# Kernel optimization log

Measured on AMD Instinct MI355X. Metric: run time of the kernel, lower is better.

The kernel has to match this reference:

```python
import jax, jax.numpy as jnp
import numpy as np

N_NODES = 50000
N_EDGES = 1600000


def setup_inputs() -> dict:
    key = jax.random.key(0)
    k1, k2, k3, k4 = jax.random.split(key, 4)
    x = jax.random.normal(k1, (N_NODES, 256), dtype=jnp.float32)
    edge_index = jax.random.randint(k2, (2, N_EDGES), 0, N_NODES, dtype=jnp.int64)
    W1 = jax.random.normal(k3, (256, 128), dtype=jnp.float32) * 0.05
    b1 = jnp.zeros((128,), dtype=jnp.float32)
    Wc = jax.random.normal(k4, (128, 10), dtype=jnp.float32) * 0.05
    bc = jnp.zeros((10,), dtype=jnp.float32)
    return {"x": x, "edge_index": edge_index, "W1": W1, "b1": b1,
            "Wc": Wc, "bc": bc, "conv_time": 30}


def reference(x, edge_index, W1, b1, Wc, bc, conv_time):
    """GCNConv(num_features->nhid) with conv_time propagation hops, ReLU, Linear cls."""
    n = x.shape[0]
    # linear transform first (standard GCNConv: transform then propagate)
    h = x @ W1 + b1  # [N, nhid]
    # add self-loops (GCN default)
    loop = jnp.arange(n, dtype=edge_index.dtype)
    src = jnp.concatenate([edge_index[0], loop])
    dst = jnp.concatenate([edge_index[1], loop])
    # symmetric normalization D^{-1/2} A_hat D^{-1/2}
    deg = jax.ops.segment_sum(jnp.ones_like(dst, dtype=h.dtype), dst, num_segments=n)
    dinv = jax.lax.rsqrt(jnp.maximum(deg, 1.0))
    norm = (dinv[src] * dinv[dst])[:, None]  # [E+N, 1]

    def hop(i, h):
        msg = h[src] * norm                      # gather + scale
        return jax.ops.segment_sum(msg, dst, num_segments=n)  # scatter-add

    h = jax.lax.fori_loop(0, conv_time, hop, h)
    h = jax.nn.relu(h)
    return h @ Wc + bc  # [N, num_classes]
```

## Files before the change

### kernel.cpp

```cpp
#include <hip/hip_runtime.h>
#include <hip/hip_bf16.h>

#define NFEAT 256
#define NHID  128
#define NCLS  10
#define CONV_TIME 30
#define NSLICE 8
#define SFEAT  16

__global__ void deg_kernel(const int* __restrict__ ei, int* __restrict__ cnt, int E) {
    int e = blockIdx.x * blockDim.x + threadIdx.x;
    if (e < E) {
        int d = ei[(size_t)E + e];
        atomicAdd(&cnt[d], 1);
    }
}

__global__ void dinv_kernel(const int* __restrict__ cnt, float* __restrict__ dinv, int n) {
    int i = blockIdx.x * blockDim.x + threadIdx.x;
    if (i < n) {
        float deg = (float)(cnt[i] + 1);
        dinv[i] = 1.0f / sqrtf(deg);
    }
}

__global__ void alloc_kernel(const int* __restrict__ cnt, int* __restrict__ alloc,
                             int* __restrict__ pbeg, int* __restrict__ plen,
                             int* __restrict__ pos, int n) {
    int i    = blockIdx.x * blockDim.x + threadIdx.x;
    int lane = threadIdx.x & 63;
    int pl   = 0;
    if (i < n) pl = (cnt[i] + 7) & ~7;
    int v = pl;
#pragma unroll
    for (int d = 1; d < 64; d <<= 1) {
        int t = __shfl_up(v, d, 64);
        if (lane >= d) v += t;
    }
    int total = __shfl(v, 63, 64);
    int excl  = v - pl;
    int base  = 0;
    if (lane == 63) base = atomicAdd(alloc, total);
    base = __shfl(base, 63, 64);
    if (i < n) {
        int seg = base + excl;
        pbeg[i] = seg;
        plen[i] = pl;
        pos[i]  = seg;
    }
}

__global__ void fill_esrc_kernel(unsigned int* __restrict__ esrc32, unsigned int val, int nwords) {
    int i = blockIdx.x * blockDim.x + threadIdx.x;
    if (i < nwords) esrc32[i] = val;
}

__global__ void scatter_kernel(const int* __restrict__ ei, int* __restrict__ pos,
                               unsigned short* __restrict__ esrc, int E) {
    int e = blockIdx.x * blockDim.x + threadIdx.x;
    if (e < E) {
        int s = ei[e];
        int d = ei[(size_t)E + e];
        int p = atomicAdd(&pos[d], 1);
        esrc[p] = (unsigned short)s;
    }
}

__global__ void init_dummy_kernel(float* __restrict__ hA, float* __restrict__ hB,
                                  int n, int np1) {
    int t = threadIdx.x;
    if (t < NSLICE * SFEAT) {
        int sl = t >> 4, f = t & 15;
        size_t idx = (size_t)sl * np1 * SFEAT + (size_t)n * SFEAT + f;
        hA[idx] = 0.0f;
        hB[idx] = 0.0f;
    }
}

__global__ __launch_bounds__(256) void gemm1_kernel(const float* __restrict__ x,
                                                    const float* __restrict__ W1,
                                                    const float* __restrict__ b1,
                                                    const float* __restrict__ dinv,
                                                    float* __restrict__ g, int M, int np1) {
    __shared__ float As[64][20];
    __shared__ float Bs[16][128];
    int tid = threadIdx.x;
    int m0  = blockIdx.x * 64;
    int tx  = tid & 15;
    int ty  = tid >> 4;
    int ar  = tid >> 2, aq = tid & 3;
    int br  = tid >> 4, bc = tid & 15;

    float acc[4][8];
#pragma unroll
    for (int i = 0; i < 4; ++i)
#pragma unroll
        for (int j = 0; j < 8; ++j) acc[i][j] = 0.0f;

    for (int kb = 0; kb < NFEAT; kb += 16) {
        float4 av = make_float4(0.f, 0.f, 0.f, 0.f);
        int arow = m0 + ar;
        if (arow < M) av = *(const float4*)(x + (size_t)arow * NFEAT + kb + aq * 4);
        *(float4*)&As[ar][aq * 4] = av;
        *(float4*)&Bs[br][bc * 8]     = *(const float4*)(W1 + (size_t)(kb + br) * NHID + bc * 8);
        *(float4*)&Bs[br][bc * 8 + 4] = *(const float4*)(W1 + (size_t)(kb + br) * NHID + bc * 8 + 4);
        __syncthreads();
#pragma unroll
        for (int k = 0; k < 16; ++k) {
            float a0 = As[ty * 4 + 0][k];
            float a1 = As[ty * 4 + 1][k];
            float a2 = As[ty * 4 + 2][k];
            float a3 = As[ty * 4 + 3][k];
            float4 b0 = *(float4*)&Bs[k][tx * 8];
            float4 b1v = *(float4*)&Bs[k][tx * 8 + 4];
            float bv[8] = {b0.x, b0.y, b0.z, b0.w, b1v.x, b1v.y, b1v.z, b1v.w};
            float avv[4] = {a0, a1, a2, a3};
#pragma unroll
            for (int i = 0; i < 4; ++i)
#pragma unroll
                for (int j = 0; j < 8; ++j)
                    acc[i][j] = fmaf(avv[i], bv[j], acc[i][j]);
        }
        __syncthreads();
    }
    int col0 = tx * 8;
    int sl   = col0 >> 4;
    int c0   = col0 & 15;
#pragma unroll
    for (int i = 0; i < 4; ++i) {
        int row = m0 + ty * 4 + i;
        if (row < M) {
            float dv = dinv[row];
            float* dst = g + (size_t)sl * np1 * SFEAT + (size_t)row * SFEAT + c0;
#pragma unroll
            for (int j = 0; j < 8; ++j)
                dst[j] = dv * (acc[i][j] + b1[col0 + j]);
        }
    }
}

__global__ __launch_bounds__(256) void hop_kernel(const float* __restrict__ gin,
                                                  float* __restrict__ gout,
                                                  const int* __restrict__ pbeg,
                                                  const int* __restrict__ plen,
                                                  const unsigned short* __restrict__ esrc,
                                                  const float* __restrict__ dinv,
                                                  int n, int np1, int last) {
    int bid  = blockIdx.x;
    int sl   = bid & (NSLICE - 1);
    int grp  = (bid >> 3) * 4 + (threadIdx.x >> 6);
    if (grp * 16 >= n) return;
    int lane = threadIdx.x & 63;
    int slot = lane >> 2;
    int fl   = lane & 3;
    int node = grp * 16 + slot;
    bool valid = node < n;
    int nodeC = valid ? node : n;
    const float4* __restrict__ gs4 = (const float4*)(gin + (size_t)sl * np1 * SFEAT);
    float4*       __restrict__ go4 = (float4*)(gout + (size_t)sl * np1 * SFEAT);

    int beg = 0, L = 0;
    if (valid) { beg = pbeg[node]; L = plen[node]; }

    float4 acc = make_float4(0.f, 0.f, 0.f, 0.f);
    const uint4* __restrict__ e4 = (const uint4*)esrc;
    for (int i = 0; i < L; i += 8) {
        uint4 w = e4[(beg + i) >> 3];
        int s0 = w.x & 0xFFFF, s1 = w.x >> 16;
        int s2 = w.y & 0xFFFF, s3 = w.y >> 16;
        int s4 = w.z & 0xFFFF, s5 = w.z >> 16;
        int s6 = w.w & 0xFFFF, s7 = w.w >> 16;
        float4 v0 = gs4[(size_t)s0 * 4 + fl];
        float4 v1 = gs4[(size_t)s1 * 4 + fl];
        float4 v2 = gs4[(size_t)s2 * 4 + fl];
        float4 v3 = gs4[(size_t)s3 * 4 + fl];
        float4 v4 = gs4[(size_t)s4 * 4 + fl];
        float4 v5 = gs4[(size_t)s5 * 4 + fl];
        float4 v6 = gs4[(size_t)s6 * 4 + fl];
        float4 v7 = gs4[(size_t)s7 * 4 + fl];
        acc.x += v0.x + v1.x + v2.x + v3.x + v4.x + v5.x + v6.x + v7.x;
        acc.y += v0.y + v1.y + v2.y + v3.y + v4.y + v5.y + v6.y + v7.y;
        acc.z += v0.z + v1.z + v2.z + v3.z + v4.z + v5.z + v6.z + v7.z;
        acc.w += v0.w + v1.w + v2.w + v3.w + v4.w + v5.w + v6.w + v7.w;
    }
    float4 sf = gs4[(size_t)nodeC * 4 + fl];
    acc.x += sf.x; acc.y += sf.y; acc.z += sf.z; acc.w += sf.w;
    float dv = valid ? dinv[node] : 1.0f;
    float sc = last ? dv : dv * dv;
    acc.x *= sc; acc.y *= sc; acc.z *= sc; acc.w *= sc;
    if (valid) go4[(size_t)node * 4 + fl] = acc;
}

__global__ __launch_bounds__(256) void cls_kernel(const float* __restrict__ h,
                                                  const float* __restrict__ Wc,
                                                  const float* __restrict__ bc,
                                                  float* __restrict__ out, int n, int np1) {
    __shared__ float wc[NHID * NCLS];
    __shared__ float bcs[NCLS];
    int tid = threadIdx.x;
    for (int i = tid; i < NHID * NCLS; i += 256) wc[i] = Wc[i];
    if (tid < NCLS) bcs[tid] = bc[tid];
    __syncthreads();
    int i = blockIdx.x * 256 + tid;
    if (i >= n) return;
    float acc[NCLS];
#pragma unroll
    for (int c = 0; c < NCLS; ++c) acc[c] = bcs[c];
#pragma unroll
    for (int s = 0; s < NSLICE; ++s) {
        const float4* hr = (const float4*)(h + ((size_t)s * np1 + i) * SFEAT);
#pragma unroll
        for (int q = 0; q < 4; ++q) {
            float4 v = hr[q];
            float vs[4] = {fmaxf(v.x, 0.f), fmaxf(v.y, 0.f), fmaxf(v.z, 0.f), fmaxf(v.w, 0.f)};
#pragma unroll
            for (int j = 0; j < 4; ++j)
#pragma unroll
                for (int c = 0; c < NCLS; ++c)
                    acc[c] = fmaf(vs[j], wc[(s * SFEAT + q * 4 + j) * NCLS + c], acc[c]);
        }
    }
#pragma unroll
    for (int c = 0; c < NCLS; ++c) out[(size_t)i * NCLS + c] = acc[c];
}

static inline size_t align256(size_t x) { return (x + 255) & ~(size_t)255; }

extern "C" void kernel_launch(void* const* d_in, const int* in_sizes, int n_in,
                              void* d_out, int out_size, void* d_ws, size_t ws_size,
                              hipStream_t stream) {
    const float* x   = (const float*)d_in[0];
    const int*   ei  = (const int*)d_in[1];
    const float* W1  = (const float*)d_in[2];
    const float* b1  = (const float*)d_in[3];
    const float* Wc  = (const float*)d_in[4];
    const float* bc  = (const float*)d_in[5];
    float*       out = (float*)d_out;

    const int N    = in_sizes[0] / NFEAT;
    const int E    = in_sizes[1] / 2;
    const int NP1  = N + 1;
    const int EPAD = E + 8 * N + 64;

    char* ws = (char*)d_ws;
    size_t off = 0;
    float*          hA   = (float*)(ws + off); off = align256(off + (size_t)NSLICE * NP1 * SFEAT * 4);
    float*          hB   = (float*)(ws + off); off = align256(off + (size_t)NSLICE * NP1 * SFEAT * 4);
    int*            cnt  = (int*)  (ws + off); off = align256(off + (size_t)(N + 64) * 4);
    float*          dinv = (float*)(ws + off); off = align256(off + (size_t)N * 4);
    int*            pbeg = (int*)  (ws + off); off = align256(off + (size_t)N * 4);
    int*            plen = (int*)  (ws + off); off = align256(off + (size_t)N * 4);
    int*            pos  = (int*)  (ws + off); off = align256(off + (size_t)N * 4);
    unsigned short* esrc = (unsigned short*)(ws + off); off = align256(off + (size_t)EPAD * 2);
    int*            alloc = cnt + N;

    hipMemsetAsync(cnt, 0, (size_t)(N + 64) * 4, stream);

    deg_kernel<<<(E + 255) / 256, 256, 0, stream>>>(ei, cnt, E);
    dinv_kernel<<<(N + 255) / 256, 256, 0, stream>>>(cnt, dinv, N);
    alloc_kernel<<<(N + 255) / 256, 256, 0, stream>>>(cnt, alloc, pbeg, plen, pos, N);
    {
        unsigned int v = ((unsigned)N << 16) | (unsigned)N;
        int nwords = EPAD / 2;
        fill_esrc_kernel<<<(nwords + 255) / 256, 256, 0, stream>>>((unsigned int*)esrc, v, nwords);
    }
    scatter_kernel<<<(E + 255) / 256, 256, 0, stream>>>(ei, pos, esrc, E);
    init_dummy_kernel<<<1, 256, 0, stream>>>(hA, hB, N, NP1);

    gemm1_kernel<<<(N + 63) / 64, 256, 0, stream>>>(x, W1, b1, dinv, hA, N, NP1);

    int ngrp = (N + 15) / 16;
    int hop_blocks = NSLICE * ((ngrp + 3) / 4);
    for (int i = 0; i < CONV_TIME; ++i) {
        const float* gi = (i & 1) ? hB : hA;
        float*       go = (i & 1) ? hA : hB;
        hop_kernel<<<hop_blocks, 256, 0, stream>>>(gi, go, pbeg, plen, esrc, dinv, N, NP1,
                                                   (i == CONV_TIME - 1) ? 1 : 0);
    }

    cls_kernel<<<(N + 255) / 256, 256, 0, stream>>>(hA, Wc, bc, out, N, NP1);
}
```

Before: 2.446 ms.

## Renumber nodes by degree bucket and partition degree/scatter atomics by destination range

Nodes are sorted into buckets by padded in-degree, and the feature buffers, CSR metadata and edge source indices are renumbered into this sorted order. The goal is that the 16 nodes sharing a wavefront in the hop kernel have similar neighbour counts, which cuts loop divergence and idle lanes across the 30 propagation hops. The final classifier writes each row back to its original node index. Separately, the degree and scatter kernels now launch 8x the blocks, and each block handles only destinations in one eighth of the node range, to localise atomics. This costs extra passes over the edge list and several small preprocessing kernels.

```diff
diff --git a/kernel.cpp b/kernel.cpp
--- a/kernel.cpp
+++ b/kernel.cpp
@@ -7,12 +7,16 @@
 #define CONV_TIME 30
 #define NSLICE 8
 #define SFEAT  16
-
-__global__ void deg_kernel(const int* __restrict__ ei, int* __restrict__ cnt, int E) {
-    int e = blockIdx.x * blockDim.x + threadIdx.x;
+#define NBUCK  32
+
+__global__ void deg_kernel(const int* __restrict__ ei, int* __restrict__ cnt, int E, int n) {
+    int part = blockIdx.x & 7;
+    int e = (blockIdx.x >> 3) * blockDim.x + threadIdx.x;
+    int lo = (int)(((long long)part * n) >> 3);
+    int hi = (int)(((long long)(part + 1) * n) >> 3);
     if (e < E) {
         int d = ei[(size_t)E + e];
-        atomicAdd(&cnt[d], 1);
+        if (d >= lo && d < hi) atomicAdd(&cnt[d], 1);
     }
 }
 
@@ -50,19 +54,84 @@
     }
 }
 
+__global__ void hist_kernel(const int* __restrict__ plen, int* __restrict__ bcnt, int n) {
+    __shared__ int lh[NBUCK];
+    int tid = threadIdx.x;
+    if (tid < NBUCK) lh[tid] = 0;
+    __syncthreads();
+    int i = blockIdx.x * blockDim.x + tid;
+    if (i < n) {
+        int b = min(plen[i] >> 3, NBUCK - 1);
+        atomicAdd(&lh[b], 1);
+    }
+    __syncthreads();
+    if (tid < NBUCK && lh[tid]) atomicAdd(&bcnt[tid], lh[tid]);
+}
+
+__global__ void scan32_kernel(const int* __restrict__ bcnt, int* __restrict__ bpos) {
+    if (threadIdx.x == 0) {
+        int a = 0;
+        for (int b = 0; b < NBUCK; ++b) { bpos[b] = a; a += bcnt[b]; }
+    }
+}
+
+__global__ void place_kernel(const int* __restrict__ plen, int* __restrict__ bpos,
+                             int* __restrict__ nperm, int* __restrict__ rank, int n) {
+    int i    = blockIdx.x * blockDim.x + threadIdx.x;
+    int lane = threadIdx.x & 63;
+    int b    = -1;
+    if (i < n) b = min(plen[i] >> 3, NBUCK - 1);
+#pragma unroll 1
+    for (int bb = 0; bb < NBUCK; ++bb) {
+        unsigned long long mask = __ballot(b == bb);
+        if (mask == 0ULL) continue;
+        int leader = __ffsll((unsigned long long)mask) - 1;
+        int cnt    = __popcll(mask);
+        int base   = 0;
+        if (lane == leader) base = atomicAdd(&bpos[bb], cnt);
+        base = __shfl(base, leader, 64);
+        int r = __popcll(mask & ((1ULL << lane) - 1ULL));
+        if (b == bb) {
+            int p = base + r;
+            nperm[p] = i;
+            rank[i]  = p;
+        }
+    }
+}
+
+__global__ void gather_sorted_kernel(const int* __restrict__ nperm,
+                                     const int* __restrict__ pbeg, const int* __restrict__ plen,
+                                     const float* __restrict__ dinv,
+                                     int* __restrict__ pbeg_s, int* __restrict__ plen_s,
+                                     float* __restrict__ dinv_s, int n) {
+    int i = blockIdx.x * blockDim.x + threadIdx.x;
+    if (i < n) {
+        int nd = nperm[i];
+        pbeg_s[i] = pbeg[nd];
+        plen_s[i] = plen[nd];
+        dinv_s[i] = dinv[nd];
+    }
+}
+
 __global__ void fill_esrc_kernel(unsigned int* __restrict__ esrc32, unsigned int val, int nwords) {
     int i = blockIdx.x * blockDim.x + threadIdx.x;
     if (i < nwords) esrc32[i] = val;
 }
 
-__global__ void scatter_kernel(const int* __restrict__ ei, int* __restrict__ pos,
-                               unsigned short* __restrict__ esrc, int E) {
-    int e = blockIdx.x * blockDim.x + threadIdx.x;
+__global__ void scatter_kernel(const int* __restrict__ ei, const int* __restrict__ rank,
+                               int* __restrict__ pos, unsigned short* __restrict__ esrc,
+                               int E, int n) {
+    int part = blockIdx.x & 7;
+    int e = (blockIdx.x >> 3) * blockDim.x + threadIdx.x;
+    int lo = (int)(((long long)part * n) >> 3);
+    int hi = (int)(((long long)(part + 1) * n) >> 3);
     if (e < E) {
-        int s = ei[e];
         int d = ei[(size_t)E + e];
-        int p = atomicAdd(&pos[d], 1);
-        esrc[p] = (unsigned short)s;
+        if (d >= lo && d < hi) {
+            int s = ei[e];
+            int p = atomicAdd(&pos[d], 1);
+            esrc[p] = (unsigned short)rank[s];
+        }
     }
 }
 
@@ -81,6 +150,7 @@
                                                     const float* __restrict__ W1,
                                                     const float* __restrict__ b1,
                                                     const float* __restrict__ dinv,
+                                                    const int* __restrict__ rank,
                                                     float* __restrict__ g, int M, int np1) {
     __shared__ float As[64][20];
     __shared__ float Bs[16][128];
@@ -131,7 +201,8 @@
         int row = m0 + ty * 4 + i;
         if (row < M) {
             float dv = dinv[row];
-            float* dst = g + (size_t)sl * np1 * SFEAT + (size_t)row * SFEAT + c0;
+            int   rk = rank[row];
+            float* dst = g + (size_t)sl * np1 * SFEAT + (size_t)rk * SFEAT + c0;
 #pragma unroll
             for (int j = 0; j < 8; ++j)
                 dst[j] = dv * (acc[i][j] + b1[col0 + j]);
@@ -141,10 +212,10 @@
 
 __global__ __launch_bounds__(256) void hop_kernel(const float* __restrict__ gin,
                                                   float* __restrict__ gout,
-                                                  const int* __restrict__ pbeg,
-                                                  const int* __restrict__ plen,
+                                                  const int* __restrict__ pbeg_s,
+                                                  const int* __restrict__ plen_s,
                                                   const unsigned short* __restrict__ esrc,
-                                                  const float* __restrict__ dinv,
+                                                  const float* __restrict__ dinv_s,
                                                   int n, int np1, int last) {
     int bid  = blockIdx.x;
     int sl   = bid & (NSLICE - 1);
@@ -153,14 +224,14 @@
     int lane = threadIdx.x & 63;
     int slot = lane >> 2;
     int fl   = lane & 3;
-    int node = grp * 16 + slot;
-    bool valid = node < n;
-    int nodeC = valid ? node : n;
+    int idx  = grp * 16 + slot;
+    bool valid = idx < n;
+    int idxC = valid ? idx : n;
     const float4* __restrict__ gs4 = (const float4*)(gin + (size_t)sl * np1 * SFEAT);
     float4*       __restrict__ go4 = (float4*)(gout + (size_t)sl * np1 * SFEAT);
 
     int beg = 0, L = 0;
-    if (valid) { beg = pbeg[node]; L = plen[node]; }
+    if (valid) { beg = pbeg_s[idx]; L = plen_s[idx]; }
 
     float4 acc = make_float4(0.f, 0.f, 0.f, 0.f);
     const uint4* __restrict__ e4 = (const uint4*)esrc;
@@ -183,17 +254,18 @@
         acc.z += v0.z + v1.z + v2.z + v3.z + v4.z + v5.z + v6.z + v7.z;
         acc.w += v0.w + v1.w + v2.w + v3.w + v4.w + v5.w + v6.w + v7.w;
     }
-    float4 sf = gs4[(size_t)nodeC * 4 + fl];
+    float4 sf = gs4[(size_t)idxC * 4 + fl];
     acc.x += sf.x; acc.y += sf.y; acc.z += sf.z; acc.w += sf.w;
-    float dv = valid ? dinv[node] : 1.0f;
+    float dv = valid ? dinv_s[idx] : 1.0f;
     float sc = last ? dv : dv * dv;
     acc.x *= sc; acc.y *= sc; acc.z *= sc; acc.w *= sc;
-    if (valid) go4[(size_t)node * 4 + fl] = acc;
+    if (valid) go4[(size_t)idx * 4 + fl] = acc;
 }
 
 __global__ __launch_bounds__(256) void cls_kernel(const float* __restrict__ h,
                                                   const float* __restrict__ Wc,
                                                   const float* __restrict__ bc,
+                                                  const int* __restrict__ nperm,
                                                   float* __restrict__ out, int n, int np1) {
     __shared__ float wc[NHID * NCLS];
     __shared__ float bcs[NCLS];
@@ -220,8 +292,9 @@
                     acc[c] = fmaf(vs[j], wc[(s * SFEAT + q * 4 + j) * NCLS + c], acc[c]);
         }
     }
-#pragma unroll
-    for (int c = 0; c < NCLS; ++c) out[(size_t)i * NCLS + c] = acc[c];
+    int nd = nperm[i];
+#pragma unroll
+    for (int c = 0; c < NCLS; ++c) out[(size_t)nd * NCLS + c] = acc[c];
 }
 
 static inline size_t align256(size_t x) { return (x + 255) & ~(size_t)255; }
@@ -244,39 +317,53 @@
 
     char* ws = (char*)d_ws;
     size_t off = 0;
-    float*          hA   = (float*)(ws + off); off = align256(off + (size_t)NSLICE * NP1 * SFEAT * 4);
-    float*          hB   = (float*)(ws + off); off = align256(off + (size_t)NSLICE * NP1 * SFEAT * 4);
-    int*            cnt  = (int*)  (ws + off); off = align256(off + (size_t)(N + 64) * 4);
-    float*          dinv = (float*)(ws + off); off = align256(off + (size_t)N * 4);
-    int*            pbeg = (int*)  (ws + off); off = align256(off + (size_t)N * 4);
-    int*            plen = (int*)  (ws + off); off = align256(off + (size_t)N * 4);
-    int*            pos  = (int*)  (ws + off); off = align256(off + (size_t)N * 4);
-    unsigned short* esrc = (unsigned short*)(ws + off); off = align256(off + (size_t)EPAD * 2);
-    int*            alloc = cnt + N;
-
-    hipMemsetAsync(cnt, 0, (size_t)(N + 64) * 4, stream);
-
-    deg_kernel<<<(E + 255) / 256, 256, 0, stream>>>(ei, cnt, E);
+    float*          hA     = (float*)(ws + off); off = align256(off + (size_t)NSLICE * NP1 * SFEAT * 4);
+    float*          hB     = (float*)(ws + off); off = align256(off + (size_t)NSLICE * NP1 * SFEAT * 4);
+    int*            cnt    = (int*)  (ws + off); off = align256(off + (size_t)(N + 256) * 4);
+    float*          dinv   = (float*)(ws + off); off = align256(off + (size_t)N * 4);
+    int*            pbeg   = (int*)  (ws + off); off = align256(off + (size_t)N * 4);
+    int*            plen   = (int*)  (ws + off); off = align256(off + (size_t)N * 4);
+    int*            pos    = (int*)  (ws + off); off = align256(off + (size_t)N * 4);
+    int*            nperm  = (int*)  (ws + off); off = align256(off + (size_t)N * 4);
+    int*            rank   = (int*)  (ws + off); off = align256(off + (size_t)N * 4);
+    int*            pbeg_s = (int*)  (ws + off); off = align256(off + (size_t)N * 4);
+    int*            plen_s = (int*)  (ws + off); off = align256(off + (size_t)N * 4);
+    float*          dinv_s = (float*)(ws + off); off = align256(off + (size_t)N * 4);
+    unsigned short* esrc   = (unsigned short*)(ws + off); off = align256(off + (size_t)EPAD * 2);
+
+    int* alloc = cnt + N;
+    int* bcnt  = cnt + N + 64;
+    int* bpos  = cnt + N + 128;
+
+    hipMemsetAsync(cnt, 0, (size_t)(N + 256) * 4, stream);
+
+    int nbE = (E + 255) / 256;
+    deg_kernel<<<8 * nbE, 256, 0, stream>>>(ei, cnt, E, N);
     dinv_kernel<<<(N + 255) / 256, 256, 0, stream>>>(cnt, dinv, N);
     alloc_kernel<<<(N + 255) / 256, 256, 0, stream>>>(cnt, alloc, pbeg, plen, pos, N);
+    hist_kernel<<<(N + 255) / 256, 256, 0, stream>>>(plen, bcnt, N);
+    scan32_kernel<<<1, 64, 0, stream>>>(bcnt, bpos);
+    place_kernel<<<(N + 255) / 256, 256, 0, stream>>>(plen, bpos, nperm, rank, N);
+    gather_sorted_kernel<<<(N + 255) / 256, 256, 0, stream>>>(nperm, pbeg, plen, dinv,
+                                                              pbeg_s, plen_s, dinv_s, N);
     {
         unsigned int v = ((unsigned)N << 16) | (unsigned)N;
         int nwords = EPAD / 2;
         fill_esrc_kernel<<<(nwords + 255) / 256, 256, 0, stream>>>((unsigned int*)esrc, v, nwords);
     }
-    scatter_kernel<<<(E + 255) / 256, 256, 0, stream>>>(ei, pos, esrc, E);
+    scatter_kernel<<<8 * nbE, 256, 0, stream>>>(ei, rank, pos, esrc, E, N);
     init_dummy_kernel<<<1, 256, 0, stream>>>(hA, hB, N, NP1);
 
-    gemm1_kernel<<<(N + 63) / 64, 256, 0, stream>>>(x, W1, b1, dinv, hA, N, NP1);
+    gemm1_kernel<<<(N + 63) / 64, 256, 0, stream>>>(x, W1, b1, dinv, rank, hA, N, NP1);
 
     int ngrp = (N + 15) / 16;
     int hop_blocks = NSLICE * ((ngrp + 3) / 4);
     for (int i = 0; i < CONV_TIME; ++i) {
         const float* gi = (i & 1) ? hB : hA;
         float*       go = (i & 1) ? hA : hB;
-        hop_kernel<<<hop_blocks, 256, 0, stream>>>(gi, go, pbeg, plen, esrc, dinv, N, NP1,
+        hop_kernel<<<hop_blocks, 256, 0, stream>>>(gi, go, pbeg_s, plen_s, esrc, dinv_s, N, NP1,
                                                    (i == CONV_TIME - 1) ? 1 : 0);
     }
 
-    cls_kernel<<<(N + 255) / 256, 256, 0, stream>>>(hA, Wc, bc, out, N, NP1);
-}
+    cls_kernel<<<(N + 255) / 256, 256, 0, stream>>>(hA, Wc, bc, nperm, out, N, NP1);
+}
```

Result: slower. 2.562 ms (+4.8%).
